# Optimization experiments

Hardware: AMD Instinct MI355X
Metric: run time of the kernel (lower is better)

Reference implementation:

```python
import jax, jax.numpy as jnp
import numpy as np

NUM_EMBEDDINGS = 1024
EMBEDDING_DIM = 64
COMMITMENT_COST = 0.25


def setup_inputs() -> dict:
    key = jax.random.key(0)
    k1, k2 = jax.random.split(key)
    inputs = jax.random.normal(k1, (64, 32, 32, EMBEDDING_DIM), dtype=jnp.float32)
    # matches nn.Embedding weight init: uniform(-1/K, 1/K)
    codebook = jax.random.uniform(
        k2, (NUM_EMBEDDINGS, EMBEDDING_DIM), dtype=jnp.float32,
        minval=-1.0 / NUM_EMBEDDINGS, maxval=1.0 / NUM_EMBEDDINGS)
    return {"inputs": inputs, "codebook": codebook}


def reference(inputs, codebook):
    input_shape = inputs.shape
    flat = inputs.reshape(-1, EMBEDDING_DIM)  # [N, D]
    distances = (jnp.sum(flat * flat, axis=1, keepdims=True)
                 + jnp.sum(codebook * codebook, axis=1)
                 - 2.0 * jnp.matmul(flat, codebook.T))
    encoding_indices = jnp.argmin(distances, axis=1)  # [N]
    quantized = codebook[encoding_indices].reshape(input_shape)
    codebook_loss = jnp.mean((jax.lax.stop_gradient(quantized) - inputs) ** 2)
    commitment_loss = jnp.mean((jax.lax.stop_gradient(inputs) - quantized) ** 2)
    vq_loss = codebook_loss + COMMITMENT_COST * commitment_loss
    # straight-through estimator
    quantized_st = inputs + jax.lax.stop_gradient(quantized - inputs)
    return quantized_st, vq_loss
```

## Files before the change

kernel.cpp:

```cpp
#include <hip/hip_runtime.h>

typedef __attribute__((ext_vector_type(8))) short short8;
typedef __attribute__((ext_vector_type(4))) float f32x4;
typedef __attribute__((ext_vector_type(4))) unsigned short u16x4;

#define NVEC 65536
#define DDIM 64
#define KCODES 1024
#define NELEM 4194304
#define VPB 64

static __device__ inline unsigned short f2bf(float f) {
  unsigned u = __builtin_bit_cast(unsigned, f);
  return (unsigned short)((u + 0x7FFFu + ((u >> 16) & 1u)) >> 16);
}
static __device__ inline float bf2f(unsigned short b) {
  return __builtin_bit_cast(float, (unsigned)b << 16);
}

__global__ __launch_bounds__(256) void vq_prep(const float* __restrict__ cb,
                                               unsigned short* __restrict__ cb_bf,
                                               float* __restrict__ en1,
                                               float* __restrict__ out) {
  int t = blockIdx.x * 256 + threadIdx.x;
  float4 v = ((const float4*)cb)[t];
  unsigned short b0 = f2bf(v.x), b1 = f2bf(v.y), b2 = f2bf(v.z), b3 = f2bf(v.w);
  u16x4 pk = {b0, b1, b2, b3};
  *(u16x4*)(cb_bf + (size_t)t * 4) = pk;
  float e0 = bf2f(b0), e1 = bf2f(b1), e2 = bf2f(b2), e3 = bf2f(b3);
  float s = (e0 * e0 + e1 * e1) + (e2 * e2 + e3 * e3);
  s += __shfl_xor(s, 1, 64);
  s += __shfl_xor(s, 2, 64);
  s += __shfl_xor(s, 4, 64);
  s += __shfl_xor(s, 8, 64);
  if ((t & 15) == 0) en1[t >> 4] = 1.0f + s;
  if (t == 0) out[NELEM] = 0.f;
}

__global__ __launch_bounds__(256, 4) void vq_main(
    const float* __restrict__ x, const float* __restrict__ cb,
    const unsigned short* __restrict__ cb_bf, const float* __restrict__ en1,
    float* __restrict__ out) {
  __shared__ float en_s[KCODES];
  __shared__ unsigned skey[VPB];
  __shared__ float xn[VPB];

  const int tid = threadIdx.x;
  const int wid = tid >> 6;
  const int L = tid & 63;
  const int c16 = L & 15;
  const int q = L >> 4;
  const int vblk = blockIdx.x * VPB;
  const int mbase = (wid & 1) * 32;
  const int cbase = (wid >> 1) * 512;

  ((float4*)en_s)[tid] = ((const float4*)en1)[tid];
  if (tid < VPB) skey[tid] = 0xFFFFFFFFu;

  short8 a[2][2];
#pragma unroll
  for (int mt = 0; mt < 2; ++mt) {
    const float* xv = x + (size_t)(vblk + mbase + mt * 16 + c16) * DDIM + q * 8;
    float4 u0 = *(const float4*)(xv);
    float4 u1 = *(const float4*)(xv + 4);
    float4 u2 = *(const float4*)(xv + 32);
    float4 u3 = *(const float4*)(xv + 36);
    unsigned short h0 = f2bf(u0.x), h1 = f2bf(u0.y), h2 = f2bf(u0.z), h3 = f2bf(u0.w);
    unsigned short h4 = f2bf(u1.x), h5 = f2bf(u1.y), h6 = f2bf(u1.z), h7 = f2bf(u1.w);
    unsigned short g0 = f2bf(u2.x), g1 = f2bf(u2.y), g2 = f2bf(u2.z), g3 = f2bf(u2.w);
    unsigned short g4 = f2bf(u3.x), g5 = f2bf(u3.y), g6 = f2bf(u3.z), g7 = f2bf(u3.w);
    short8 A0 = {(short)h0, (short)h1, (short)h2, (short)h3,
                 (short)h4, (short)h5, (short)h6, (short)h7};
    short8 A1 = {(short)g0, (short)g1, (short)g2, (short)g3,
                 (short)g4, (short)g5, (short)g6, (short)g7};
    a[mt][0] = A0;
    a[mt][1] = A1;
    float s0 = bf2f(h0), s1 = bf2f(h1), s2 = bf2f(h2), s3 = bf2f(h3);
    float s4 = bf2f(h4), s5 = bf2f(h5), s6 = bf2f(h6), s7 = bf2f(h7);
    float t0 = bf2f(g0), t1 = bf2f(g1), t2 = bf2f(g2), t3 = bf2f(g3);
    float t4 = bf2f(g4), t5 = bf2f(g5), t6 = bf2f(g6), t7 = bf2f(g7);
    float xs = ((s0 * s0 + s1 * s1) + (s2 * s2 + s3 * s3)) +
               ((s4 * s4 + s5 * s5) + (s6 * s6 + s7 * s7)) +
               ((t0 * t0 + t1 * t1) + (t2 * t2 + t3 * t3)) +
               ((t4 * t4 + t5 * t5) + (t6 * t6 + t7 * t7));
    xs += __shfl_xor(xs, 16, 64);
    xs += __shfl_xor(xs, 32, 64);
    if (wid < 2 && L < 16) xn[mbase + mt * 16 + L] = xs;
  }
  __syncthreads();

  unsigned bestk[2][4];
#pragma unroll
  for (int m = 0; m < 2; ++m)
#pragma unroll
    for (int r = 0; r < 4; ++r) bestk[m][r] = 0xFFFFFFFFu;

  const unsigned short* bptr = cb_bf + (size_t)(cbase + c16) * DDIM + q * 8;
#pragma unroll 4
  for (int nt = 0; nt < 32; ++nt) {
    short8 b0 = *(const short8*)(bptr + nt * 16 * DDIM);
    short8 b1 = *(const short8*)(bptr + nt * 16 * DDIM + 32);
    float env = en_s[cbase + nt * 16 + c16];
    unsigned kidx = (unsigned)(cbase + nt * 16 + c16);
#pragma unroll
    for (int m = 0; m < 2; ++m) {
      f32x4 z = {0.f, 0.f, 0.f, 0.f};
      f32x4 acc = __builtin_amdgcn_mfma_f32_16x16x32_bf16(a[m][0], b0, z, 0, 0, 0);
      acc = __builtin_amdgcn_mfma_f32_16x16x32_bf16(a[m][1], b1, acc, 0, 0, 0);
#pragma unroll
      for (int r = 0; r < 4; ++r) {
        float p = fmaf(-2.f, acc[r], env);
        unsigned key = (__builtin_bit_cast(unsigned, p) & 0xFFFFFC00u) | kidx;
        bestk[m][r] = key < bestk[m][r] ? key : bestk[m][r];
      }
    }
  }

#pragma unroll
  for (int m = 0; m < 2; ++m)
#pragma unroll
    for (int r = 0; r < 4; ++r) {
      unsigned k = bestk[m][r];
      k = min(k, (unsigned)__shfl_xor((int)k, 1, 64));
      k = min(k, (unsigned)__shfl_xor((int)k, 2, 64));
      k = min(k, (unsigned)__shfl_xor((int)k, 4, 64));
      k = min(k, (unsigned)__shfl_xor((int)k, 8, 64));
      if (c16 == 0) atomicMin(&skey[mbase + m * 16 + q * 4 + r], k);
    }
  __syncthreads();

#pragma unroll
  for (int i = 0; i < 4; ++i) {
    int f = i * 256 + tid;
    int v = f >> 4, d4 = f & 15;
    int id = (int)(skey[v] & 1023u);
    ((float4*)out)[(size_t)vblk * 16 + f] = ((const float4*)cb)[(size_t)id * 16 + d4];
  }

  if (wid == 0) {
    unsigned k = skey[L];
    float pt = __builtin_bit_cast(float, k & 0xFFFFFC00u);
    float pl = (pt - 1.0f) + xn[L];
#pragma unroll
    for (int off = 32; off >= 1; off >>= 1) pl += __shfl_down(pl, off, 64);
    if (L == 0) atomicAdd(out + NELEM, pl * (1.25f / (float)NELEM));
  }
}

extern "C" void kernel_launch(void* const* d_in, const int* in_sizes, int n_in,
                              void* d_out, int out_size, void* d_ws,
                              size_t ws_size, hipStream_t stream) {
  const float* x = (const float*)d_in[0];
  const float* cb = (const float*)d_in[1];
  float* out = (float*)d_out;
  char* ws = (char*)d_ws;
  unsigned short* cb_bf = (unsigned short*)ws;
  float* en1 = (float*)(ws + 131072);

  vq_prep<<<64, 256, 0, stream>>>(cb, cb_bf, en1, out);
  vq_main<<<NVEC / VPB, 256, 0, stream>>>(x, cb, cb_bf, en1, out);
}
```

Measured before the change: 115.5 us.

## Enlarge block tile to 128 vectors, share A fragments via LDS, prefetch codebook

Each block now handles 128 input vectors, and each wave covers all 128 rows against its own 256-code slice instead of 32 rows against 512 codes. The bf16 A fragments are staged through shared memory so every wave can hold all eight row tiles in registers. Codebook fragment loads are software-pipelined one step ahead. This aims to reuse each codebook load across four times as many MFMAs and cut total codebook traffic, at the cost of much higher register pressure (occupancy hint lowered from 4 to 2 blocks) and fewer, larger blocks.

```diff
diff --git a/kernel.cpp b/kernel.cpp
--- a/kernel.cpp
+++ b/kernel.cpp
@@ -8,7 +8,10 @@
 #define DDIM 64
 #define KCODES 1024
 #define NELEM 4194304
-#define VPB 64
+#define VPB 128
+#define MT 8
+#define CW 256
+#define NT (CW / 16)
 
 static __device__ inline unsigned short f2bf(float f) {
   unsigned u = __builtin_bit_cast(unsigned, f);
@@ -37,10 +40,11 @@
   if (t == 0) out[NELEM] = 0.f;
 }
 
-__global__ __launch_bounds__(256, 4) void vq_main(
+__global__ __launch_bounds__(256, 2) void vq_main(
     const float* __restrict__ x, const float* __restrict__ cb,
     const unsigned short* __restrict__ cb_bf, const float* __restrict__ en1,
     float* __restrict__ out) {
+  __shared__ alignas(16) unsigned short xs[MT * 2 * 64 * 8];
   __shared__ float en_s[KCODES];
   __shared__ unsigned skey[VPB];
   __shared__ float xn[VPB];
@@ -51,16 +55,15 @@
   const int c16 = L & 15;
   const int q = L >> 4;
   const int vblk = blockIdx.x * VPB;
-  const int mbase = (wid & 1) * 32;
-  const int cbase = (wid >> 1) * 512;
+  const int cbase = wid * CW;
 
   ((float4*)en_s)[tid] = ((const float4*)en1)[tid];
   if (tid < VPB) skey[tid] = 0xFFFFFFFFu;
 
-  short8 a[2][2];
 #pragma unroll
-  for (int mt = 0; mt < 2; ++mt) {
-    const float* xv = x + (size_t)(vblk + mbase + mt * 16 + c16) * DDIM + q * 8;
+  for (int half_i = 0; half_i < 2; ++half_i) {
+    const int mt = wid * 2 + half_i;
+    const float* xv = x + (size_t)(vblk + mt * 16 + c16) * DDIM + q * 8;
     float4 u0 = *(const float4*)(xv);
     float4 u1 = *(const float4*)(xv + 4);
     float4 u2 = *(const float4*)(xv + 32);
@@ -69,41 +72,57 @@
     unsigned short h4 = f2bf(u1.x), h5 = f2bf(u1.y), h6 = f2bf(u1.z), h7 = f2bf(u1.w);
     unsigned short g0 = f2bf(u2.x), g1 = f2bf(u2.y), g2 = f2bf(u2.z), g3 = f2bf(u2.w);
     unsigned short g4 = f2bf(u3.x), g5 = f2bf(u3.y), g6 = f2bf(u3.z), g7 = f2bf(u3.w);
-    short8 A0 = {(short)h0, (short)h1, (short)h2, (short)h3,
-                 (short)h4, (short)h5, (short)h6, (short)h7};
-    short8 A1 = {(short)g0, (short)g1, (short)g2, (short)g3,
-                 (short)g4, (short)g5, (short)g6, (short)g7};
-    a[mt][0] = A0;
-    a[mt][1] = A1;
+    u16x4 p0 = {h0, h1, h2, h3}, p1 = {h4, h5, h6, h7};
+    u16x4 p2 = {g0, g1, g2, g3}, p3 = {g4, g5, g6, g7};
+    unsigned short* l0 = xs + ((size_t)(mt * 2 + 0) * 64 + L) * 8;
+    unsigned short* l1 = xs + ((size_t)(mt * 2 + 1) * 64 + L) * 8;
+    *(u16x4*)(l0) = p0;
+    *(u16x4*)(l0 + 4) = p1;
+    *(u16x4*)(l1) = p2;
+    *(u16x4*)(l1 + 4) = p3;
     float s0 = bf2f(h0), s1 = bf2f(h1), s2 = bf2f(h2), s3 = bf2f(h3);
     float s4 = bf2f(h4), s5 = bf2f(h5), s6 = bf2f(h6), s7 = bf2f(h7);
-    float t0 = bf2f(g0), t1 = bf2f(g1), t2 = bf2f(g2), t3 = bf2f(g3);
-    float t4 = bf2f(g4), t5 = bf2f(g5), t6 = bf2f(g6), t7 = bf2f(g7);
-    float xs = ((s0 * s0 + s1 * s1) + (s2 * s2 + s3 * s3)) +
+    float w0 = bf2f(g0), w1 = bf2f(g1), w2 = bf2f(g2), w3 = bf2f(g3);
+    float w4 = bf2f(g4), w5 = bf2f(g5), w6 = bf2f(g6), w7 = bf2f(g7);
+    float sx = ((s0 * s0 + s1 * s1) + (s2 * s2 + s3 * s3)) +
                ((s4 * s4 + s5 * s5) + (s6 * s6 + s7 * s7)) +
-               ((t0 * t0 + t1 * t1) + (t2 * t2 + t3 * t3)) +
-               ((t4 * t4 + t5 * t5) + (t6 * t6 + t7 * t7));
-    xs += __shfl_xor(xs, 16, 64);
-    xs += __shfl_xor(xs, 32, 64);
-    if (wid < 2 && L < 16) xn[mbase + mt * 16 + L] = xs;
+               ((w0 * w0 + w1 * w1) + (w2 * w2 + w3 * w3)) +
+               ((w4 * w4 + w5 * w5) + (w6 * w6 + w7 * w7));
+    sx += __shfl_xor(sx, 16, 64);
+    sx += __shfl_xor(sx, 32, 64);
+    if (L < 16) xn[mt * 16 + L] = sx;
   }
   __syncthreads();
 
-  unsigned bestk[2][4];
+  short8 a[MT][2];
 #pragma unroll
-  for (int m = 0; m < 2; ++m)
+  for (int m = 0; m < MT; ++m) {
+    a[m][0] = *(const short8*)(xs + ((m * 2 + 0) * 64 + L) * 8);
+    a[m][1] = *(const short8*)(xs + ((m * 2 + 1) * 64 + L) * 8);
+  }
+
+  unsigned bestk[MT][4];
+#pragma unroll
+  for (int m = 0; m < MT; ++m)
 #pragma unroll
     for (int r = 0; r < 4; ++r) bestk[m][r] = 0xFFFFFFFFu;
 
-  const unsigned short* bptr = cb_bf + (size_t)(cbase + c16) * DDIM + q * 8;
-#pragma unroll 4
-  for (int nt = 0; nt < 32; ++nt) {
-    short8 b0 = *(const short8*)(bptr + nt * 16 * DDIM);
-    short8 b1 = *(const short8*)(bptr + nt * 16 * DDIM + 32);
-    float env = en_s[cbase + nt * 16 + c16];
+  const unsigned short* bp = cb_bf + (size_t)(cbase + c16) * DDIM + q * 8;
+  short8 nb0 = *(const short8*)(bp);
+  short8 nb1 = *(const short8*)(bp + 32);
+  float nenv = en_s[cbase + c16];
+#pragma unroll
+  for (int nt = 0; nt < NT; ++nt) {
+    short8 b0 = nb0, b1 = nb1;
+    float env = nenv;
+    if (nt < NT - 1) {
+      nb0 = *(const short8*)(bp + (nt + 1) * 16 * DDIM);
+      nb1 = *(const short8*)(bp + (nt + 1) * 16 * DDIM + 32);
+      nenv = en_s[cbase + (nt + 1) * 16 + c16];
+    }
     unsigned kidx = (unsigned)(cbase + nt * 16 + c16);
 #pragma unroll
-    for (int m = 0; m < 2; ++m) {
+    for (int m = 0; m < MT; ++m) {
       f32x4 z = {0.f, 0.f, 0.f, 0.f};
       f32x4 acc = __builtin_amdgcn_mfma_f32_16x16x32_bf16(a[m][0], b0, z, 0, 0, 0);
       acc = __builtin_amdgcn_mfma_f32_16x16x32_bf16(a[m][1], b1, acc, 0, 0, 0);
@@ -117,7 +136,7 @@
   }
 
 #pragma unroll
-  for (int m = 0; m < 2; ++m)
+  for (int m = 0; m < MT; ++m)
 #pragma unroll
     for (int r = 0; r < 4; ++r) {
       unsigned k = bestk[m][r];
@@ -125,22 +144,23 @@
       k = min(k, (unsigned)__shfl_xor((int)k, 2, 64));
       k = min(k, (unsigned)__shfl_xor((int)k, 4, 64));
       k = min(k, (unsigned)__shfl_xor((int)k, 8, 64));
-      if (c16 == 0) atomicMin(&skey[mbase + m * 16 + q * 4 + r], k);
+      if (c16 == 0) atomicMin(&skey[m * 16 + q * 4 + r], k);
     }
   __syncthreads();
 
 #pragma unroll
-  for (int i = 0; i < 4; ++i) {
+  for (int i = 0; i < 8; ++i) {
     int f = i * 256 + tid;
     int v = f >> 4, d4 = f & 15;
     int id = (int)(skey[v] & 1023u);
     ((float4*)out)[(size_t)vblk * 16 + f] = ((const float4*)cb)[(size_t)id * 16 + d4];
   }
 
-  if (wid == 0) {
-    unsigned k = skey[L];
+  if (wid < 2) {
+    int vslot = wid * 64 + L;
+    unsigned k = skey[vslot];
     float pt = __builtin_bit_cast(float, k & 0xFFFFFC00u);
-    float pl = (pt - 1.0f) + xn[L];
+    float pl = (pt - 1.0f) + xn[vslot];
 #pragma unroll
     for (int off = 32; off >= 1; off >>= 1) pl += __shfl_down(pl, off, 64);
     if (L == 0) atomicAdd(out + NELEM, pl * (1.25f / (float)NELEM));
```

New measurement: 184.5 us. 1.6x slower.
